# Performance work log

Hardware: AMD Instinct MI355X
Metric: run time of the kernel (lower is better)

The kernel has to match this reference:

```python
import jax, jax.numpy as jnp
import numpy as np

B, S, H = 2, 2048, 2048
NH, NKV, HD = 16, 4, 128
GROUPS = NH // NKV
THETA = 10000.0
EPS = 1e-6


def setup_inputs() -> dict:
    key = jax.random.key(0)
    ks = jax.random.split(key, 6)
    scale = 0.02
    return {
        "hidden_states": jax.random.normal(ks[0], (B, S, H), jnp.float32),
        "wq": jax.random.normal(ks[1], (NH * HD, H), jnp.float32) * scale,
        "wk": jax.random.normal(ks[2], (NKV * HD, H), jnp.float32) * scale,
        "wv": jax.random.normal(ks[3], (NKV * HD, H), jnp.float32) * scale,
        "wo": jax.random.normal(ks[4], (H, NH * HD), jnp.float32) * scale,
        "q_norm_weight": jnp.ones((HD,), jnp.float32),
        "k_norm_weight": jnp.ones((HD,), jnp.float32),
    }


def _rope_tables(seq_len):
    inv_freq = 1.0 / (THETA ** (jnp.arange(0, HD, 2, dtype=jnp.float32) / HD))
    t = jnp.arange(seq_len, dtype=jnp.float32)
    freqs = jnp.outer(t, inv_freq)              # [S, HD/2]
    emb = jnp.concatenate([freqs, freqs], -1)   # [S, HD]
    return jnp.cos(emb), jnp.sin(emb)


def _rotate_half(x):
    x1, x2 = x[..., : HD // 2], x[..., HD // 2:]
    return jnp.concatenate([-x2, x1], -1)


def _rmsnorm(x, w):
    var = jnp.mean(jnp.square(x), axis=-1, keepdims=True)
    return x * jax.lax.rsqrt(var + EPS) * w


def reference(hidden_states, wq, wk, wv, wo, q_norm_weight, k_norm_weight):
    b, s, _ = hidden_states.shape
    q = (hidden_states @ wq.T).reshape(b, s, NH, HD).transpose(0, 2, 1, 3)    # [b,nh,s,d]
    k = (hidden_states @ wk.T).reshape(b, s, NKV, HD).transpose(0, 2, 1, 3)   # [b,nkv,s,d]
    v = (hidden_states @ wv.T).reshape(b, s, NKV, HD).transpose(0, 2, 1, 3)

    cos, sin = _rope_tables(s)                  # [s,d]
    q = q * cos + _rotate_half(q) * sin
    k = k * cos + _rotate_half(k) * sin

    # fused QK RMSNorm (applied inside fused_qknorm_flash_attention)
    q = _rmsnorm(q, q_norm_weight)
    k = _rmsnorm(k, k_norm_weight)

    # GQA: share each kv head across GROUPS query heads without materializing repeats
    qg = q.reshape(b, NKV, GROUPS, s, HD)
    scale = 1.0 / jnp.sqrt(jnp.float32(HD))
    scores = jnp.einsum('bhgqd,bhkd->bhgqk', qg, k) * scale   # [b,nkv,g,s,s]
    causal = jnp.tril(jnp.ones((s, s), bool))
    scores = jnp.where(causal, scores, jnp.finfo(scores.dtype).min)
    probs = jax.nn.softmax(scores, axis=-1)
    out = jnp.einsum('bhgqk,bhkd->bhgqd', probs, v)            # [b,nkv,g,s,d]
    out = out.reshape(b, NH, s, HD).transpose(0, 2, 1, 3).reshape(b, s, NH * HD)
    return out @ wo.T
```

## Files before the change

### kernel.cpp

```cpp
#include <hip/hip_runtime.h>
#include <math.h>

typedef __bf16 bf16;
typedef __bf16 bf16x8 __attribute__((ext_vector_type(8)));
typedef __bf16 bf16x4 __attribute__((ext_vector_type(4)));
typedef float f32x4 __attribute__((ext_vector_type(4)));

#define B_DIM 2
#define S_LEN 2048
#define H_DIM 2048
#define NH 16
#define NKV 4
#define HD 128

__device__ __forceinline__ void gl_lds16(const void* g, void* l) {
    __builtin_amdgcn_global_load_lds(
        (const __attribute__((address_space(1))) unsigned int*)g,
        (__attribute__((address_space(3))) unsigned int*)l, 16, 0, 0);
}

__device__ __forceinline__ void bar() {
    asm volatile("" ::: "memory");
    __builtin_amdgcn_s_barrier();
    asm volatile("" ::: "memory");
}

__global__ __launch_bounds__(256) void cast_all(const float* __restrict__ s0,
                                                const float* __restrict__ s1,
                                                const float* __restrict__ s2,
                                                const float* __restrict__ s3,
                                                const float* __restrict__ s4,
                                                bf16* __restrict__ dst) {
    const int i = blockIdx.x * 256 + threadIdx.x;
    const float* src;
    int off;
    if (i < 2097152)      { src = s0; off = 0; }
    else if (i < 3145728) { src = s1; off = 2097152; }
    else if (i < 3407872) { src = s2; off = 3145728; }
    else if (i < 3670016) { src = s3; off = 3407872; }
    else                  { src = s4; off = 3670016; }
    float4 f = ((const float4*)src)[i - off];
    bf16x4 o = { (bf16)f.x, (bf16)f.y, (bf16)f.z, (bf16)f.w };
    *(bf16x4*)(dst + (size_t)i * 4) = o;
}

template <typename OutT>
__global__ __launch_bounds__(512, 2) void gemm256(const bf16* __restrict__ A,
                                                  const bf16* __restrict__ Bt,
                                                  OutT* __restrict__ C,
                                                  int M, int N, int K) {
    __shared__ __align__(16) bf16 smem[65536];
    const int t = threadIdx.x, lane = t & 63, w = t >> 6;
    const int lr = lane & 15, quad = lane >> 4;
    const int nN = N >> 8;
    const int nwg = gridDim.x, chunk = nwg >> 3;
    const int bid = blockIdx.x;
    const int lid = (bid & 7) * chunk + (bid >> 3);
    const int m0 = (lid / nN) << 8, n0 = (lid % nN) << 8;
    const int mh_w = w >> 2;
    const int wn = (w & 3) << 6;
    const int nh_w = (w & 3) >> 1;
    const int rb = (w & 1) << 6;
    const int nK = K >> 6;

    const int ld0 = w * 2;
    const int lrow = lane >> 2;
    const int csrc = (lane & 3) ^ ((lane >> 3) & 3);
    const int swz = (lr >> 1) & 3;

    auto stA = [&](int ts, int mh) {
        if (ts < nK) {
            bf16* db = smem + (ts & 1) * 16384 + mh * 8192;
            const bf16* sp = A + (size_t)(m0 + mh * 128) * K + ts * 64;
#pragma unroll
            for (int i = 0; i < 2; i++) {
                const int ldi = ld0 + i, kb = ldi >> 3, rg = ldi & 7;
                gl_lds16(sp + (size_t)(rg * 16 + lrow) * K + kb * 32 + csrc * 8,
                         db + kb * 4096 + rg * 512);
            }
        }
    };
    auto stB = [&](int ts, int nh) {
        if (ts < nK) {
            bf16* db = smem + 32768 + (ts & 1) * 16384 + nh * 8192;
            const bf16* sp = Bt + (size_t)(n0 + nh * 128) * K + ts * 64;
#pragma unroll
            for (int i = 0; i < 2; i++) {
                const int ldi = ld0 + i, kb = ldi >> 3, rg = ldi & 7;
                gl_lds16(sp + (size_t)(rg * 16 + lrow) * K + kb * 32 + csrc * 8,
                         db + kb * 4096 + rg * 512);
            }
        }
    };

    f32x4 acc[8][4];
#pragma unroll
    for (int i = 0; i < 8; i++)
#pragma unroll
        for (int j = 0; j < 4; j++) acc[i][j] = (f32x4){0.f, 0.f, 0.f, 0.f};
    bf16x8 af[8], b0[4], b1[4];

    auto rdA = [&](int s, int fi0) {
        const bf16* bp = smem + s * 16384 + mh_w * 8192;
#pragma unroll
        for (int f = 0; f < 4; f++)
#pragma unroll
            for (int ks = 0; ks < 2; ks++)
                af[f * 2 + ks] = *(const bf16x8*)(bp + ks * 4096 +
                                                  ((fi0 + f) * 16 + lr) * 32 + (quad ^ swz) * 8);
    };
    auto rdB = [&](int s, int fj0, bf16x8* dst) {
        const bf16* bp = smem + 32768 + s * 16384 + nh_w * 8192;
#pragma unroll
        for (int f = 0; f < 2; f++)
#pragma unroll
            for (int ks = 0; ks < 2; ks++)
                dst[f * 2 + ks] = *(const bf16x8*)(bp + ks * 4096 +
                                                   (rb + (fj0 + f) * 16 + lr) * 32 + (quad ^ swz) * 8);
    };
    auto mm16 = [&](int fi0, int fj0, bf16x8* bb) {
        __builtin_amdgcn_s_setprio(1);
#pragma unroll
        for (int f = 0; f < 4; f++)
#pragma unroll
            for (int g = 0; g < 2; g++)
#pragma unroll
                for (int ks = 0; ks < 2; ks++)
                    acc[fi0 + f][fj0 + g] = __builtin_amdgcn_mfma_f32_16x16x32_bf16(
                        af[f * 2 + ks], bb[g * 2 + ks], acc[fi0 + f][fj0 + g], 0, 0, 0);
        __builtin_amdgcn_s_setprio(0);
    };

    stA(0, 0); stA(0, 1); stB(0, 0); stB(0, 1); stA(1, 0);
    asm volatile("s_waitcnt vmcnt(2)" ::: "memory");
    bar();

    for (int ts = 0; ts < nK; ++ts) {
        const int s = ts & 1;
        rdA(s, 0); rdB(s, 0, b0);
        stA(ts + 1, 1);
        bar();
        mm16(0, 0, b0);
        bar();
        rdB(s, 2, b1);
        stB(ts + 1, 0);
        bar();
        mm16(0, 2, b1);
        bar();
        rdA(s, 4);
        stB(ts + 1, 1);
        bar();
        mm16(4, 2, b1);
        bar();
        rdB(s, 0, b0);
        stA(ts + 2, 0);
        bar();
        mm16(4, 0, b0);
        if (ts + 2 < nK) asm volatile("s_waitcnt vmcnt(2)" ::: "memory");
        else             asm volatile("s_waitcnt vmcnt(0)" ::: "memory");
        bar();
    }
#pragma unroll
    for (int fi = 0; fi < 8; fi++) {
        const int m = m0 + mh_w * 128 + fi * 16 + quad * 4;
#pragma unroll
        for (int fj = 0; fj < 4; fj++) {
            const int n = n0 + wn + fj * 16 + lr;
#pragma unroll
            for (int r = 0; r < 4; r++)
                C[(size_t)(m + r) * N + n] = (OutT)acc[fi][fj][r];
        }
    }
}

__global__ __launch_bounds__(512, 1) void gemm_pn(const bf16* __restrict__ A,
                                                  const bf16* __restrict__ Bt,
                                                  float* __restrict__ C,
                                                  int M, int N, int K) {
    __shared__ __align__(16) bf16 smem[49152];
    const int t = threadIdx.x, lane = t & 63, w = t >> 6;
    const int lr = lane & 15, quad = lane >> 4;
    const int nN = N >> 7;
    const int nwg = gridDim.x, chunk = nwg >> 3;
    const int bid = blockIdx.x;
    const int lid = (bid & 7) * chunk + (bid >> 3);
    const int m0 = (lid / nN) << 8, n0 = (lid % nN) << 7;
    const int mh_w = w >> 2;
    const int wn = (w & 3) << 5;
    const int nK = K >> 6;

    const int ld0 = w * 2;
    const int lrow = lane >> 2;
    const int csrc = (lane & 3) ^ ((lane >> 3) & 3);
    const int swz = (lr >> 1) & 3;

    auto stA = [&](int ts, int mh) {
        if (ts < nK) {
            bf16* db = smem + (ts & 1) * 16384 + mh * 8192;
            const bf16* sp = A + (size_t)(m0 + mh * 128) * K + ts * 64;
#pragma unroll
            for (int i = 0; i < 2; i++) {
                const int ldi = ld0 + i, kb = ldi >> 3, rg = ldi & 7;
                gl_lds16(sp + (size_t)(rg * 16 + lrow) * K + kb * 32 + csrc * 8,
                         db + kb * 4096 + rg * 512);
            }
        }
    };
    auto stB1 = [&](int ts) {
        if (ts < nK) {
            bf16* db = smem + 32768 + (ts & 1) * 8192;
            const bf16* sp = Bt + (size_t)n0 * K + ts * 64;
#pragma unroll
            for (int i = 0; i < 2; i++) {
                const int ldi = ld0 + i, kb = ldi >> 3, rg = ldi & 7;
                gl_lds16(sp + (size_t)(rg * 16 + lrow) * K + kb * 32 + csrc * 8,
                         db + kb * 4096 + rg * 512);
            }
        }
    };

    f32x4 acc[8][2];
#pragma unroll
    for (int i = 0; i < 8; i++)
#pragma unroll
        for (int j = 0; j < 2; j++) acc[i][j] = (f32x4){0.f, 0.f, 0.f, 0.f};
    bf16x8 af[8], bf1[4];

    auto rdA = [&](int s, int fi0) {
        const bf16* bp = smem + s * 16384 + mh_w * 8192;
#pragma unroll
        for (int f = 0; f < 4; f++)
#pragma unroll
            for (int ks = 0; ks < 2; ks++)
                af[f * 2 + ks] = *(const bf16x8*)(bp + ks * 4096 +
                                                  ((fi0 + f) * 16 + lr) * 32 + (quad ^ swz) * 8);
    };
    auto rdB1 = [&](int s) {
        const bf16* bp = smem + 32768 + s * 8192;
#pragma unroll
        for (int f = 0; f < 2; f++)
#pragma unroll
            for (int ks = 0; ks < 2; ks++)
                bf1[f * 2 + ks] = *(const bf16x8*)(bp + ks * 4096 +
                                                   (wn + f * 16 + lr) * 32 + (quad ^ swz) * 8);
    };
    auto mm8 = [&](int fi0, int ks) {
        __builtin_amdgcn_s_setprio(1);
#pragma unroll
        for (int f = 0; f < 4; f++)
#pragma unroll
            for (int g = 0; g < 2; g++)
                acc[fi0 + f][g] = __builtin_amdgcn_mfma_f32_16x16x32_bf16(
                    af[f * 2 + ks], bf1[g * 2 + ks], acc[fi0 + f][g], 0, 0, 0);
        __builtin_amdgcn_s_setprio(0);
    };

    stA(0, 0); stA(0, 1); stB1(0);
    asm volatile("s_waitcnt vmcnt(0)" ::: "memory");
    bar();

    for (int ts = 0; ts < nK; ++ts) {
        const int s = ts & 1;
        rdA(s, 0); rdB1(s);
        stA(ts + 1, 0);
        bar();
        mm8(0, 0);
        bar();
        stA(ts + 1, 1);
        stB1(ts + 1);
        bar();
        mm8(0, 1);
        bar();
        rdA(s, 4);
        bar();
        mm8(4, 0);
        bar();
        mm8(4, 1);
        asm volatile("s_waitcnt vmcnt(0)" ::: "memory");
        bar();
    }
#pragma unroll
    for (int fi = 0; fi < 8; fi++) {
        const int m = m0 + mh_w * 128 + fi * 16 + quad * 4;
#pragma unroll
        for (int fj = 0; fj < 2; fj++) {
            const int n = n0 + wn + fj * 16 + lr;
#pragma unroll
            for (int r = 0; r < 4; r++)
                C[(size_t)(m + r) * N + n] = acc[fi][fj][r];
        }
    }
}

__global__ __launch_bounds__(256) void rope_rms(const bf16* __restrict__ qkv,
                                                const float* __restrict__ qw,
                                                const float* __restrict__ kw,
                                                bf16* __restrict__ qb,
                                                bf16* __restrict__ kb,
                                                bf16* __restrict__ vt) {
    const int tok = blockIdx.x;
    const int b = tok >> 11, s = tok & (S_LEN - 1);
    const int lane = threadIdx.x & 63, w = threadIdx.x >> 6;
    const bf16* row = qkv + (size_t)tok * 3072;
    const float inv = expf(-(float)lane * (9.210340371976184f / 64.f));
    const float ang = (float)s * inv;
    float s_, c_;
    sincosf(ang, &s_, &c_);
    const float wq1 = qw[lane], wq2 = qw[lane + 64];
    const float wk1 = kw[lane], wk2 = kw[lane + 64];
    for (int u = w; u < 24; u += 4) {
        if (u < 16) {
            const float x1 = (float)row[u * 128 + lane], x2 = (float)row[u * 128 + 64 + lane];
            float y1 = x1 * c_ - x2 * s_;
            float y2 = x2 * c_ + x1 * s_;
            float ss = y1 * y1 + y2 * y2;
#pragma unroll
            for (int m = 1; m < 64; m <<= 1) ss += __shfl_xor(ss, m);
            const float r = rsqrtf(ss * (1.f / 128.f) + 1e-6f);
            size_t o = ((size_t)(b * NH + u) * S_LEN + s) * HD;
            qb[o + lane]      = (bf16)(y1 * r * wq1);
            qb[o + 64 + lane] = (bf16)(y2 * r * wq2);
        } else if (u < 20) {
            const int kh = u - 16;
            const float x1 = (float)row[2048 + kh * 128 + lane], x2 = (float)row[2048 + kh * 128 + 64 + lane];
            float y1 = x1 * c_ - x2 * s_;
            float y2 = x2 * c_ + x1 * s_;
            float ss = y1 * y1 + y2 * y2;
#pragma unroll
            for (int m = 1; m < 64; m <<= 1) ss += __shfl_xor(ss, m);
            const float r = rsqrtf(ss * (1.f / 128.f) + 1e-6f);
            size_t base = (size_t)(b * NKV + kh) * 16 * 16384;
            kb[base + (size_t)(lane >> 3) * 16384 + s * 8 + (lane & 7)]       = (bf16)(y1 * r * wk1);
            kb[base + (size_t)(8 + (lane >> 3)) * 16384 + s * 8 + (lane & 7)] = (bf16)(y2 * r * wk2);
        } else {
            const int vh = u - 20;
            const float x1 = (float)row[2560 + vh * 128 + lane], x2 = (float)row[2560 + vh * 128 + 64 + lane];
            const int m = s & 31;
            const int gi = (s >> 5) * 4 + ((m & 15) >> 2);
            const int el = ((m >> 4) << 2) | (m & 3);
            size_t base = ((size_t)(b * NKV + vh) * 256 + gi) * 1024 + el;
            vt[base + (size_t)lane * 8]        = (bf16)x1;
            vt[base + (size_t)(lane + 64) * 8] = (bf16)x2;
        }
    }
}

__global__ __launch_bounds__(256, 3) void flash(const bf16* __restrict__ qg,
                                                const bf16* __restrict__ kg,
                                                const bf16* __restrict__ vg,
                                                bf16* __restrict__ attn,
                                                float* __restrict__ part_o,
                                                float* __restrict__ part_l) {
    static const unsigned char QT[22] = {9,8,15,15,7,14,14,13,13,6,12,12,11,11,5,10,10,4,3,2,1,0};
    static const unsigned char CK[22] = {2,2,0,1,2,0,1,0,1,2,0,1,0,1,2,0,1,2,2,2,2,2};
    const int idx = blockIdx.x;
    const int g = idx >> 5, hb = idx & 31;
    const int qt = QT[g], ck = CK[g];
    const int h = hb & 15, b = hb >> 4;
    const int kvh = h >> 2;
    const int ktBeg = (ck == 1) ? (qt + 1) : 0;
    const int ktEnd = (ck == 0) ? (qt + 1) : (2 * qt + 2);
    const bf16* qh = qg + (size_t)(b * NH + h) * S_LEN * HD;
    const bf16* kh = kg + (size_t)(b * NKV + kvh) * (16 * 16384);
    const bf16* vh = vg + (size_t)(b * NKV + kvh) * (256 * 1024);
    __shared__ __align__(16) bf16 Ks[2][16 * 512];
    __shared__ __align__(16) bf16 Vs[8 * 1024];
    const int t = threadIdx.x, lane = t & 63, w = t >> 6, lr = lane & 15, quad = lane >> 4;
    const int row0 = qt * 128 + w * 32;
    bf16x8 qf[2][4];
#pragma unroll
    for (int mg = 0; mg < 2; mg++)
#pragma unroll
        for (int c = 0; c < 4; c++)
            qf[mg][c] = *(const bf16x8*)(qh + (size_t)(row0 + mg * 16 + lr) * HD + c * 32 + quad * 8);
    f32x4 o[2][8];
    f32x4 lacc[2];
#pragma unroll
    for (int mg = 0; mg < 2; mg++) {
        lacc[mg] = (f32x4){0.f, 0.f, 0.f, 0.f};
#pragma unroll
        for (int j = 0; j < 8; j++) o[mg][j] = (f32x4){0.f, 0.f, 0.f, 0.f};
    }
    const bf16 one = (bf16)1.0f;
    const bf16x8 ones8 = {one, one, one, one, one, one, one, one};
    const float C1 = 0.12751744f;
    const float C2 = -17.3123405f;

    auto stageK = [&](int kt_) {
        if (kt_ < ktEnd) {
            bf16* dst = Ks[kt_ & 1];
            const int kb = kt_ * 64;
#pragma unroll
            for (int i = 0; i < 4; i++) {
                const int dc = w * 4 + i;
                gl_lds16(kh + (size_t)dc * 16384 + (size_t)kb * 8 + lane * 8, dst + dc * 512);
            }
        }
    };
    auto stageV = [&](int kt_) {
#pragma unroll
        for (int i = 0; i < 2; i++) {
            const int c = w * 2 + i;
            const bf16* src = vh + (size_t)(8 * kt_ + c) * 1024 + lane * 8;
            gl_lds16(src, &Vs[c * 1024]);
            gl_lds16(src + 512, &Vs[c * 1024 + 512]);
        }
    };

    stageK(ktBeg);
    stageK(ktBeg + 1);
    __syncthreads();

    for (int kt = ktBeg; kt < ktEnd; ++kt) {
        const int kbase = kt * 64;
        const int cur = kt & 1;
        stageV(kt);
        f32x4 sacc[2][4];
#pragma unroll
        for (int mg = 0; mg < 2; mg++)
#pragma unroll
            for (int n = 0; n < 4; n++) sacc[mg][n] = (f32x4){0.f, 0.f, 0.f, 0.f};
#pragma unroll
        for (int c = 0; c < 4; c++)
#pragma unroll
            for (int n = 0; n < 4; n++) {
                bf16x8 kf = *(const bf16x8*)&Ks[cur][(c * 4 + quad) * 512 + (n * 16 + lr) * 8];
                sacc[0][n] = __builtin_amdgcn_mfma_f32_16x16x32_bf16(kf, qf[0][c], sacc[0][n], 0, 0, 0);
                sacc[1][n] = __builtin_amdgcn_mfma_f32_16x16x32_bf16(kf, qf[1][c], sacc[1][n], 0, 0, 0);
            }
        const bool diag = (kt >= 2 * qt);
        bf16x8 pT[2][2];
#pragma unroll
        for (int mg = 0; mg < 2; mg++) {
            const int qrow = row0 + mg * 16 + lr;
#pragma unroll
            for (int n = 0; n < 4; n++)
#pragma unroll
                for (int r = 0; r < 4; r++) {
                    float ev = exp2f(fmaf(sacc[mg][n][r], C1, C2));
                    if (diag) {
                        const int key = kbase + n * 16 + quad * 4 + r;
                        ev = (key <= qrow) ? ev : 0.f;
                    }
                    pT[mg][n >> 1][(n & 1) * 4 + r] = (bf16)ev;
                }
        }
        asm volatile("s_waitcnt vmcnt(0)" ::: "memory");
        bar();
        stageK(kt + 2);
#pragma unroll
        for (int k2 = 0; k2 < 2; k2++) {
#pragma unroll
            for (int j = 0; j < 8; j++) {
                bf16x8 vf = *(const bf16x8*)&Vs[(k2 * 4 + quad) * 1024 + (j * 16 + lr) * 8];
                o[0][j] = __builtin_amdgcn_mfma_f32_16x16x32_bf16(vf, pT[0][k2], o[0][j], 0, 0, 0);
                o[1][j] = __builtin_amdgcn_mfma_f32_16x16x32_bf16(vf, pT[1][k2], o[1][j], 0, 0, 0);
            }
            lacc[0] = __builtin_amdgcn_mfma_f32_16x16x32_bf16(ones8, pT[0][k2], lacc[0], 0, 0, 0);
            lacc[1] = __builtin_amdgcn_mfma_f32_16x16x32_bf16(ones8, pT[1][k2], lacc[1], 0, 0, 0);
        }
        bar();
    }
    if (ck == 2) {
#pragma unroll
        for (int mg = 0; mg < 2; mg++) {
            const float inv = 1.0f / lacc[mg][0];
            const int qrow = row0 + mg * 16 + lr;
            bf16* dst = attn + ((size_t)(b * S_LEN) + qrow) * (NH * HD) + h * HD + quad * 4;
#pragma unroll
            for (int j = 0; j < 8; j++) {
                bf16x4 st = { (bf16)(o[mg][j][0] * inv), (bf16)(o[mg][j][1] * inv),
                              (bf16)(o[mg][j][2] * inv), (bf16)(o[mg][j][3] * inv) };
                *(bf16x4*)(dst + j * 16) = st;
            }
        }
    } else {
        const int slot = ((b * NH + h) * 6 + (qt - 10)) * 2 + ck;
        float* po = part_o + (size_t)slot * 16384;
#pragma unroll
        for (int mg = 0; mg < 2; mg++) {
            const int row = w * 32 + mg * 16 + lr;
#pragma unroll
            for (int j = 0; j < 8; j++) {
                float4 st = { o[mg][j][0], o[mg][j][1], o[mg][j][2], o[mg][j][3] };
                *(float4*)(po + row * 128 + j * 16 + quad * 4) = st;
            }
            if (quad == 0) part_l[slot * 128 + row] = lacc[mg][0];
        }
    }
}

__global__ __launch_bounds__(256) void reduce_attn(const float* __restrict__ part_o,
                                                   const float* __restrict__ part_l,
                                                   bf16* __restrict__ attn) {
    const int blk = blockIdx.x;
    const int qt = (blk % 6) + 10;
    const int h = (blk / 6) & 15, b = blk / 96;
    const float* p0 = part_o + (size_t)(blk * 2 + 0) * 16384;
    const float* p1 = part_o + (size_t)(blk * 2 + 1) * 16384;
    const float* l0 = part_l + (blk * 2 + 0) * 128;
    const float* l1 = part_l + (blk * 2 + 1) * 128;
    const int t = threadIdx.x;
#pragma unroll
    for (int it = 0; it < 16; it++) {
        const int idx = it * 256 + t;
        const int row = idx >> 5, d4 = idx & 31;
        float4 a = ((const float4*)p0)[idx];
        float4 c = ((const float4*)p1)[idx];
        const float inv = 1.0f / (l0[row] + l1[row]);
        bf16x4 ov = { (bf16)((a.x + c.x) * inv), (bf16)((a.y + c.y) * inv),
                      (bf16)((a.z + c.z) * inv), (bf16)((a.w + c.w) * inv) };
        *(bf16x4*)(attn + ((size_t)(b * S_LEN) + qt * 128 + row) * (NH * HD) + h * HD + d4 * 4) = ov;
    }
}

extern "C" void kernel_launch(void* const* d_in, const int* in_sizes, int n_in,
                              void* d_out, int out_size, void* d_ws, size_t ws_size,
                              hipStream_t stream) {
    (void)in_sizes; (void)n_in; (void)out_size; (void)ws_size;
    const float* hs  = (const float*)d_in[0];
    const float* wq  = (const float*)d_in[1];
    const float* wk  = (const float*)d_in[2];
    const float* wv  = (const float*)d_in[3];
    const float* wo  = (const float*)d_in[4];
    const float* qnw = (const float*)d_in[5];
    const float* knw = (const float*)d_in[6];
    float* out = (float*)d_out;

    char* ws = (char*)d_ws;
    size_t off = 0;
    auto alloc = [&](size_t bytes) {
        void* p = ws + off;
        off += (bytes + 255) & ~(size_t)255;
        return p;
    };
    bf16* hs_bf   = (bf16*)alloc((size_t)4096 * 2048 * 2);
    bf16* wqkv_bf = (bf16*)alloc((size_t)3072 * 2048 * 2);
    bf16* wo_bf   = (bf16*)alloc((size_t)2048 * 2048 * 2);
    bf16* qkv_bf  = (bf16*)alloc((size_t)4096 * 3072 * 2);
    bf16* q_bf    = (bf16*)alloc((size_t)B_DIM * NH * S_LEN * HD * 2);
    bf16* k_bf    = (bf16*)alloc((size_t)B_DIM * NKV * S_LEN * HD * 2);
    bf16* vt_bf   = (bf16*)alloc((size_t)B_DIM * NKV * S_LEN * HD * 2);
    bf16* at_bf   = (bf16*)alloc((size_t)4096 * 2048 * 2);

    float* part_o = (float*)hs_bf;
    float* part_l = (float*)((char*)hs_bf + (size_t)384 * 16384 * 4);

    cast_all<<<18432, 256, 0, stream>>>(hs, wq, wk, wv, wo, hs_bf);
    gemm256<bf16><<<dim3(192), 512, 0, stream>>>(hs_bf, wqkv_bf, qkv_bf, 4096, 3072, 2048);
    rope_rms<<<4096, 256, 0, stream>>>(qkv_bf, qnw, knw, q_bf, k_bf, vt_bf);
    flash<<<dim3(704), 256, 0, stream>>>(q_bf, k_bf, vt_bf, at_bf, part_o, part_l);
    reduce_attn<<<dim3(192), 256, 0, stream>>>(part_o, part_l, at_bf);
    gemm_pn<<<dim3(256), 512, 0, stream>>>(at_bf, wo_bf, out, 4096, 2048, 2048);
}
```

Baseline: 307.6 us.

## Double-buffer V tiles alongside K with a single barrier per iteration

V moves into a double buffer next to K, and both tiles for the next key block are prefetched at the start of each iteration. This replaces the old scheme, where V was loaded and waited on mid-iteration and K was prefetched two ahead. The mid-loop vmcnt wait and barrier are removed, leaving one __syncthreads per iteration. LDS use rises from 48KB to 64KB per block, so launch bounds drop from 3 to 2 blocks per CU, which cuts occupancy.

Result: no change. 309.6 us (+0.7%).

```diff
diff --git a/kernel.cpp b/kernel.cpp
--- a/kernel.cpp
+++ b/kernel.cpp
@@ -345,7 +345,7 @@
     }
 }
 
-__global__ __launch_bounds__(256, 3) void flash(const bf16* __restrict__ qg,
+__global__ __launch_bounds__(256, 2) void flash(const bf16* __restrict__ qg,
                                                 const bf16* __restrict__ kg,
                                                 const bf16* __restrict__ vg,
                                                 bf16* __restrict__ attn,
@@ -364,7 +364,7 @@
     const bf16* kh = kg + (size_t)(b * NKV + kvh) * (16 * 16384);
     const bf16* vh = vg + (size_t)(b * NKV + kvh) * (256 * 1024);
     __shared__ __align__(16) bf16 Ks[2][16 * 512];
-    __shared__ __align__(16) bf16 Vs[8 * 1024];
+    __shared__ __align__(16) bf16 Vs[2][8 * 1024];
     const int t = threadIdx.x, lane = t & 63, w = t >> 6, lr = lane & 15, quad = lane >> 4;
     const int row0 = qt * 128 + w * 32;
     bf16x8 qf[2][4];
@@ -386,35 +386,29 @@
     const float C1 = 0.12751744f;
     const float C2 = -17.3123405f;
 
-    auto stageK = [&](int kt_) {
-        if (kt_ < ktEnd) {
-            bf16* dst = Ks[kt_ & 1];
-            const int kb = kt_ * 64;
-#pragma unroll
-            for (int i = 0; i < 4; i++) {
-                const int dc = w * 4 + i;
-                gl_lds16(kh + (size_t)dc * 16384 + (size_t)kb * 8 + lane * 8, dst + dc * 512);
-            }
-        }
-    };
-    auto stageV = [&](int kt_) {
+    auto stage = [&](int kt_, int bi) {
+        const int kb = kt_ * 64;
+#pragma unroll
+        for (int i = 0; i < 4; i++) {
+            const int dc = w * 4 + i;
+            gl_lds16(kh + (size_t)dc * 16384 + (size_t)kb * 8 + lane * 8, &Ks[bi][dc * 512]);
+        }
 #pragma unroll
         for (int i = 0; i < 2; i++) {
             const int c = w * 2 + i;
             const bf16* src = vh + (size_t)(8 * kt_ + c) * 1024 + lane * 8;
-            gl_lds16(src, &Vs[c * 1024]);
-            gl_lds16(src + 512, &Vs[c * 1024 + 512]);
-        }
-    };
-
-    stageK(ktBeg);
-    stageK(ktBeg + 1);
+            gl_lds16(src, &Vs[bi][c * 1024]);
+            gl_lds16(src + 512, &Vs[bi][c * 1024 + 512]);
+        }
+    };
+
+    stage(ktBeg, 0);
     __syncthreads();
+    int cur = 0;
 
     for (int kt = ktBeg; kt < ktEnd; ++kt) {
         const int kbase = kt * 64;
-        const int cur = kt & 1;
-        stageV(kt);
+        if (kt + 1 < ktEnd) stage(kt + 1, cur ^ 1);
         f32x4 sacc[2][4];
 #pragma unroll
         for (int mg = 0; mg < 2; mg++)
@@ -445,21 +439,19 @@
                     pT[mg][n >> 1][(n & 1) * 4 + r] = (bf16)ev;
                 }
         }
-        asm volatile("s_waitcnt vmcnt(0)" ::: "memory");
-        bar();
-        stageK(kt + 2);
 #pragma unroll
         for (int k2 = 0; k2 < 2; k2++) {
 #pragma unroll
             for (int j = 0; j < 8; j++) {
-                bf16x8 vf = *(const bf16x8*)&Vs[(k2 * 4 + quad) * 1024 + (j * 16 + lr) * 8];
+                bf16x8 vf = *(const bf16x8*)&Vs[cur][(k2 * 4 + quad) * 1024 + (j * 16 + lr) * 8];
                 o[0][j] = __builtin_amdgcn_mfma_f32_16x16x32_bf16(vf, pT[0][k2], o[0][j], 0, 0, 0);
                 o[1][j] = __builtin_amdgcn_mfma_f32_16x16x32_bf16(vf, pT[1][k2], o[1][j], 0, 0, 0);
             }
             lacc[0] = __builtin_amdgcn_mfma_f32_16x16x32_bf16(ones8, pT[0][k2], lacc[0], 0, 0, 0);
             lacc[1] = __builtin_amdgcn_mfma_f32_16x16x32_bf16(ones8, pT[1][k2], lacc[1], 0, 0, 0);
         }
-        bar();
+        __syncthreads();
+        cur ^= 1;
     }
     if (ck == 2) {
 #pragma unroll
```
